# Kernel tuning notes

Hardware: AMD Instinct MI355X
Metric: run time of the kernel (lower is better)

The kernel has to match this reference:

```python
import jax, jax.numpy as jnp
import numpy as np

NUM_CLASSES = 5
NUM_THRESHOLDS = NUM_CLASSES - 1  # 4
B = 8388608

def setup_inputs() -> dict:
    key = jax.random.key(0)
    k1, k2 = jax.random.split(key)
    logits = jax.random.normal(k1, (B, NUM_THRESHOLDS), dtype=jnp.float32)
    targets = jax.random.randint(k2, (B,), 0, NUM_CLASSES, dtype=jnp.int64)
    return {"logits": logits, "targets": targets}

def reference(logits, targets):
    # ordinal_targets[i, j] = 1.0 if j < targets[i] else 0.0
    thr = jnp.arange(NUM_THRESHOLDS, dtype=targets.dtype)  # (T,)
    ordinal_targets = (thr[None, :] < targets[:, None]).astype(logits.dtype)  # (B, T)
    # BCE with logits: max(x,0) - x*y + log(1+exp(-|x|)) (numerically stable)
    x = logits
    loss = jnp.maximum(x, 0.0) - x * ordinal_targets + jnp.log1p(jnp.exp(-jnp.abs(x)))
    return loss.mean()
```

## Files before the change

### kernel.cpp

```cpp
#include <hip/hip_runtime.h>


#define NROWS 8388608
#define NTHR 4

__device__ __forceinline__ float bce_term(float x, int j, int tgt) {
    float y = (j < tgt) ? 1.0f : 0.0f;
    return fmaxf(x, 0.0f) - x * y + __logf(1.0f + __expf(-fabsf(x)));
}

__global__ __launch_bounds__(256) void ord_loss_reduce(
        const float4* __restrict__ logits4,
        const int* __restrict__ targets,
        double* __restrict__ ws_sum,
        int nrows) {
    int tid = blockIdx.x * blockDim.x + threadIdx.x;
    int stride = gridDim.x * blockDim.x;

    float acc = 0.0f;
    for (int i = tid; i < nrows; i += stride) {
        float4 x = logits4[i];
        int t = targets[i];
        acc += bce_term(x.x, 0, t);
        acc += bce_term(x.y, 1, t);
        acc += bce_term(x.z, 2, t);
        acc += bce_term(x.w, 3, t);
    }

    #pragma unroll
    for (int off = 32; off > 0; off >>= 1)
        acc += __shfl_down(acc, off, 64);

    __shared__ float wsum[4];
    int lane = threadIdx.x & 63;
    int wid  = threadIdx.x >> 6;
    if (lane == 0) wsum[wid] = acc;
    __syncthreads();

    if (threadIdx.x == 0) {
        float s = wsum[0] + wsum[1] + wsum[2] + wsum[3];
        atomicAdd(ws_sum, (double)s);
    }
}

__global__ void ord_loss_final(const double* __restrict__ ws_sum,
                               float* __restrict__ out) {
    out[0] = (float)(ws_sum[0] * (1.0 / ((double)NROWS * (double)NTHR)));
}

extern "C" void kernel_launch(void* const* d_in, const int* in_sizes, int n_in,
                              void* d_out, int out_size, void* d_ws, size_t ws_size,
                              hipStream_t stream) {
    const float4* logits = (const float4*)d_in[0];
    const int* targets = (const int*)d_in[1];
    double* ws_sum = (double*)d_ws;
    float* out = (float*)d_out;

    hipMemsetAsync(ws_sum, 0, sizeof(double), stream);

    int nrows = NROWS;
    int block = 256;
    int grid = 2048;
    ord_loss_reduce<<<grid, block, 0, stream>>>(logits, targets, ws_sum, nrows);
    ord_loss_final<<<1, 1, 0, stream>>>(ws_sum, out);
}
```

Before: 221.5 us.

## Unroll grid-stride loop with batched loads and replace atomics with partials reduction

```diff
diff --git a/kernel.cpp b/kernel.cpp
--- a/kernel.cpp
+++ b/kernel.cpp
@@ -2,50 +2,83 @@
 
 
 #define NROWS 8388608
-#define NTHR 4
+#define NTHR  4
+#define BLOCK 256
+#define GRID  2048
+#define NTHREADS (BLOCK * GRID)
+#define RPT   (NROWS / NTHREADS)
 
-__device__ __forceinline__ float bce_term(float x, int j, int tgt) {
-    float y = (j < tgt) ? 1.0f : 0.0f;
-    return fmaxf(x, 0.0f) - x * y + __logf(1.0f + __expf(-fabsf(x)));
+__device__ __forceinline__ float row_loss(float4 x, int t) {
+    float s0 = fmaxf(x.x, 0.f) + __logf(1.f + __expf(-fabsf(x.x))) - (t > 0 ? x.x : 0.f);
+    float s1 = fmaxf(x.y, 0.f) + __logf(1.f + __expf(-fabsf(x.y))) - (t > 1 ? x.y : 0.f);
+    float s2 = fmaxf(x.z, 0.f) + __logf(1.f + __expf(-fabsf(x.z))) - (t > 2 ? x.z : 0.f);
+    float s3 = fmaxf(x.w, 0.f) + __logf(1.f + __expf(-fabsf(x.w))) - (t > 3 ? x.w : 0.f);
+    return (s0 + s1) + (s2 + s3);
 }
 
-__global__ __launch_bounds__(256) void ord_loss_reduce(
+__global__ __launch_bounds__(BLOCK) void ord_loss_reduce(
         const float4* __restrict__ logits4,
-        const int* __restrict__ targets,
-        double* __restrict__ ws_sum,
-        int nrows) {
-    int tid = blockIdx.x * blockDim.x + threadIdx.x;
-    int stride = gridDim.x * blockDim.x;
+        const int*    __restrict__ targets,
+        float*        __restrict__ partials) {
+    const int tid = blockIdx.x * BLOCK + threadIdx.x;
 
     float acc = 0.0f;
-    for (int i = tid; i < nrows; i += stride) {
-        float4 x = logits4[i];
-        int t = targets[i];
-        acc += bce_term(x.x, 0, t);
-        acc += bce_term(x.y, 1, t);
-        acc += bce_term(x.z, 2, t);
-        acc += bce_term(x.w, 3, t);
+    #pragma unroll
+    for (int c = 0; c < RPT / 4; ++c) {
+        const int i0 = tid + (4 * c + 0) * NTHREADS;
+        const int i1 = tid + (4 * c + 1) * NTHREADS;
+        const int i2 = tid + (4 * c + 2) * NTHREADS;
+        const int i3 = tid + (4 * c + 3) * NTHREADS;
+        float4 x0 = logits4[i0];
+        float4 x1 = logits4[i1];
+        float4 x2 = logits4[i2];
+        float4 x3 = logits4[i3];
+        int t0 = targets[i0];
+        int t1 = targets[i1];
+        int t2 = targets[i2];
+        int t3 = targets[i3];
+        acc += row_loss(x0, t0);
+        acc += row_loss(x1, t1);
+        acc += row_loss(x2, t2);
+        acc += row_loss(x3, t3);
     }
 
     #pragma unroll
     for (int off = 32; off > 0; off >>= 1)
         acc += __shfl_down(acc, off, 64);
 
-    __shared__ float wsum[4];
-    int lane = threadIdx.x & 63;
-    int wid  = threadIdx.x >> 6;
+    __shared__ float wsum[BLOCK / 64];
+    const int lane = threadIdx.x & 63;
+    const int wid  = threadIdx.x >> 6;
     if (lane == 0) wsum[wid] = acc;
     __syncthreads();
 
-    if (threadIdx.x == 0) {
-        float s = wsum[0] + wsum[1] + wsum[2] + wsum[3];
-        atomicAdd(ws_sum, (double)s);
-    }
+    if (threadIdx.x == 0)
+        partials[blockIdx.x] = (wsum[0] + wsum[1]) + (wsum[2] + wsum[3]);
 }
 
-__global__ void ord_loss_final(const double* __restrict__ ws_sum,
-                               float* __restrict__ out) {
-    out[0] = (float)(ws_sum[0] * (1.0 / ((double)NROWS * (double)NTHR)));
+__global__ __launch_bounds__(BLOCK) void ord_loss_final(
+        const float* __restrict__ partials,
+        float*       __restrict__ out) {
+    double a = 0.0;
+    #pragma unroll
+    for (int k = 0; k < GRID / BLOCK; ++k)
+        a += (double)partials[threadIdx.x + k * BLOCK];
+
+    #pragma unroll
+    for (int off = 32; off > 0; off >>= 1)
+        a += __shfl_down(a, off, 64);
+
+    __shared__ double wsum[BLOCK / 64];
+    const int lane = threadIdx.x & 63;
+    const int wid  = threadIdx.x >> 6;
+    if (lane == 0) wsum[wid] = a;
+    __syncthreads();
+
+    if (threadIdx.x == 0) {
+        double total = (wsum[0] + wsum[1]) + (wsum[2] + wsum[3]);
+        out[0] = (float)(total / ((double)NROWS * (double)NTHR));
+    }
 }
 
 extern "C" void kernel_launch(void* const* d_in, const int* in_sizes, int n_in,
@@ -53,14 +86,9 @@
                               hipStream_t stream) {
     const float4* logits = (const float4*)d_in[0];
     const int* targets = (const int*)d_in[1];
-    double* ws_sum = (double*)d_ws;
+    float* partials = (float*)d_ws;
     float* out = (float*)d_out;
 
-    hipMemsetAsync(ws_sum, 0, sizeof(double), stream);
-
-    int nrows = NROWS;
-    int block = 256;
-    int grid = 2048;
-    ord_loss_reduce<<<grid, block, 0, stream>>>(logits, targets, ws_sum, nrows);
-    ord_loss_final<<<1, 1, 0, stream>>>(ws_sum, out);
+    ord_loss_reduce<<<GRID, BLOCK, 0, stream>>>(logits, targets, partials);
+    ord_loss_final<<<1, BLOCK, 0, stream>>>(partials, out);
 }
```

Result: faster. 212.0 us (-4.3%).
